# Optimization experiments

Measured on AMD Instinct MI355X. Metric: run time of the kernel, lower is better.

## Reference

```python
import jax, jax.numpy as jnp
import numpy as np

D = 256
H = 1024
N_TAU = 10  # steps per delay interval; dt = tau / N_TAU (matches dt = 0.1*tau in source)


def setup_inputs() -> dict:
    key = jax.random.key(0)
    k1, k2, k3, k4 = jax.random.split(key, 4)
    x_0 = jax.random.normal(k1, (D,), dtype=jnp.float32)
    # Small weight scales keep the explicit Euler DDE solve numerically tame over 10k steps
    W1 = jax.random.normal(k2, (H, 2 * D), dtype=jnp.float32) * 0.05
    b1 = jax.random.normal(k3, (H,), dtype=jnp.float32) * 0.05
    W2 = jax.random.normal(k4, (D, H), dtype=jnp.float32) * 0.002
    b2 = jnp.zeros((D,), dtype=jnp.float32)
    return {"x_0": x_0, "W1": W1, "b1": b1, "W2": W2, "b2": b2, "tau": 1, "T": 1000}


def reference(x_0, W1, b1, W2, b2, tau, T):
    # DDE: x'(t) = F(x(t), x(t - tau), t) for t in [0, T]; x(t) = x_0 for t in [-tau, 0].
    # Solver: explicit Euler with dt = tau / N_tau, N = floor(T / dt) steps.
    dt = 0.1 * float(tau)
    N = int(np.floor(float(T) / dt))

    def F(x, y, t):
        # MODEL: one-hidden-layer tanh MLP on concat(x(t), x(t - tau))
        h = jnp.tanh(W1 @ jnp.concatenate([x, y]) + b1)
        return W2 @ h + b2

    # Rolling buffer of the last N_tau states; history x(t) = x_0 for t <= 0.
    buf0 = jnp.broadcast_to(x_0, (N_TAU, D))  # buf[0] == x[j - N_tau]

    def step(carry, t):
        x, buf = carry
        y = buf[0]                     # delayed state x(t - tau)
        x_new = x + dt * F(x, y, t)
        buf_new = jnp.concatenate([buf[1:], x[None, :]], axis=0)
        return (x_new, buf_new), x_new

    ts = jnp.arange(N, dtype=jnp.float32) * dt
    (_, _), xs = jax.lax.scan(step, (x_0, buf0), ts)  # xs: [N, d]
    traj = jnp.concatenate([x_0[None, :], xs], axis=0)  # [N+1, d]
    return traj.T  # [d, N+1]: kth column = state at kth time step
```

## Files before the change

kernel.cpp:

```cpp
#include <hip/hip_runtime.h>
#include <math.h>


#define NTAU 10
#define DD   256
#define HH   1024
#define NWG  32
#define TPB  256
#define HPW  (HH / NWG)
#define KPT  64

__global__ __launch_bounds__(TPB, 1)
void ndde_persist(const float* __restrict__ x0,
                  const float* __restrict__ W1,
                  const float* __restrict__ b1,
                  const float* __restrict__ W2,
                  const float* __restrict__ b2,
                  const int*   __restrict__ taup,
                  float* __restrict__ out,
                  float*        P,
                  unsigned int* ctr,
                  int N)
{
    const int w  = blockIdx.x;
    const int t  = threadIdx.x;
    const int r  = t >> 3;
    const int i  = t & 7;
    const int row  = w * HPW + r;
    const int col0 = w * HPW;

    const float dt = 0.1f * (float)(*taup);

    __shared__ __align__(16) float xcur[DD];
    __shared__ __align__(16) float hist[NTAU][DD];
    __shared__ __align__(16) float hsh[HPW];

    float4 w1r[16];
    {
        const float* wrow = W1 + (size_t)row * (2 * DD);
        #pragma unroll
        for (int j = 0; j < 16; ++j) {
            int jj = (j + i) & 15;
            w1r[j] = *(const float4*)(wrow + i * KPT + 4 * jj);
        }
    }
    float4 w2r[8];
    #pragma unroll
    for (int c = 0; c < 8; ++c)
        w2r[c] = *(const float4*)(W2 + (size_t)t * HH + col0 + 4 * c);

    const float b1r = b1[row];
    const float b2r = b2[t];
    const float x0r = x0[t];
    const bool  writer = (r == w);
    float* orow = out + (size_t)t * (N + 1);

    xcur[t] = x0r;
    #pragma unroll
    for (int q = 0; q < NTAU; ++q) hist[q][t] = x0r;
    if (writer) orow[0] = x0r;
    __syncthreads();

    int hidx = 0;
    for (int s = 0; s < N; ++s) {
        const float* zbase = (i < 4) ? (xcur + (i & 3) * KPT)
                                     : (hist[hidx] + (i & 3) * KPT);
        float ax = 0.f, ay = 0.f, az = 0.f, aw = 0.f;
        #pragma unroll
        for (int j = 0; j < 16; ++j) {
            int jj = (j + i) & 15;
            float4 zv = *(const float4*)(zbase + 4 * jj);
            float4 wv = w1r[j];
            ax = fmaf(wv.x, zv.x, ax);
            ay = fmaf(wv.y, zv.y, ay);
            az = fmaf(wv.z, zv.z, az);
            aw = fmaf(wv.w, zv.w, aw);
        }
        float acc = (ax + ay) + (az + aw);
        acc += __shfl_xor(acc, 1);
        acc += __shfl_xor(acc, 2);
        acc += __shfl_xor(acc, 4);
        if (i == 0) hsh[r] = tanhf(acc + b1r);
        __syncthreads();

        float px = 0.f, py = 0.f, pz = 0.f, pw = 0.f;
        #pragma unroll
        for (int c = 0; c < 8; ++c) {
            float4 hv = *(const float4*)(&hsh[4 * c]);
            float4 wv = w2r[c];
            px = fmaf(wv.x, hv.x, px);
            py = fmaf(wv.y, hv.y, py);
            pz = fmaf(wv.z, hv.z, pz);
            pw = fmaf(wv.w, hv.w, pw);
        }
        float p = (px + py) + (pz + pw);

        float* slot = P + ((size_t)(s & 1) * NWG + w) * DD;
        __hip_atomic_store(slot + t, p, __ATOMIC_RELAXED, __HIP_MEMORY_SCOPE_AGENT);
        __syncthreads();

        if (t == 0) {
            __hip_atomic_fetch_add(ctr, 1u, __ATOMIC_RELAXED, __HIP_MEMORY_SCOPE_AGENT);
            const unsigned int target = (unsigned int)(s + 1) * NWG;
            while (__hip_atomic_load(ctr, __ATOMIC_RELAXED, __HIP_MEMORY_SCOPE_AGENT) < target)
                __builtin_amdgcn_s_sleep(1);
        }
        __syncthreads();

        float* gp = P + (size_t)(s & 1) * NWG * DD + t;
        float delta = 0.f;
        #pragma unroll
        for (int ww = 0; ww < NWG; ++ww)
            delta += __hip_atomic_load(gp + (size_t)ww * DD, __ATOMIC_RELAXED,
                                       __HIP_MEMORY_SCOPE_AGENT);

        const float xold = xcur[t];
        const float xnew = fmaf(dt, delta + b2r, xold);
        hist[hidx][t] = xold;
        xcur[t]       = xnew;
        if (writer) orow[s + 1] = xnew;
        hidx = (hidx + 1 == NTAU) ? 0 : hidx + 1;
        __syncthreads();
    }
}

extern "C" void kernel_launch(void* const* d_in, const int* in_sizes, int n_in,
                              void* d_out, int out_size, void* d_ws, size_t ws_size,
                              hipStream_t stream)
{
    const float* x0  = (const float*)d_in[0];
    const float* W1  = (const float*)d_in[1];
    const float* b1  = (const float*)d_in[2];
    const float* W2  = (const float*)d_in[3];
    const float* b2  = (const float*)d_in[4];
    const int*  taup = (const int*)d_in[5];

    const int Dv = in_sizes[0];
    const int N  = out_size / Dv - 1;

    unsigned int* ctr = (unsigned int*)d_ws;
    float* P = (float*)((char*)d_ws + 256);

    hipMemsetAsync(d_ws, 0, 256, stream);

    hipLaunchKernelGGL(ndde_persist, dim3(NWG), dim3(TPB), 0, stream,
                       x0, W1, b1, W2, b2, taup,
                       (float*)d_out, P, ctr, N);
}
```

Measured before the change: 28.50 ms.

## Replace global atomic counter barrier with step-tagged 64-bit partial slots

Each partial sum is now stored packed with its step number in a 64-bit word. Readers spin on the tags of all 32 slots directly instead of waiting on a fetch-add counter barrier and extra __syncthreads. This removes the serialized atomic counter, the single-thread spin, and two workgroup barriers per step. In exchange every thread polls 32 remote slots, and slots are never cleared between launches, so stale tags from an earlier call could match and be read as valid data.

Result: slower. 75.43 ms (+164.7%).

```diff
diff --git a/kernel.cpp b/kernel.cpp
--- a/kernel.cpp
+++ b/kernel.cpp
@@ -10,6 +10,9 @@
 #define HPW  (HH / NWG)
 #define KPT  64
 
+typedef unsigned long long u64;
+typedef unsigned int       u32;
+
 __global__ __launch_bounds__(TPB, 1)
 void ndde_persist(const float* __restrict__ x0,
                   const float* __restrict__ W1,
@@ -18,8 +21,7 @@
                   const float* __restrict__ b2,
                   const int*   __restrict__ taup,
                   float* __restrict__ out,
-                  float*        P,
-                  unsigned int* ctr,
+                  u64*          P,
                   int N)
 {
     const int w  = blockIdx.x;
@@ -95,24 +97,27 @@
         }
         float p = (px + py) + (pz + pw);
 
-        float* slot = P + ((size_t)(s & 1) * NWG + w) * DD;
-        __hip_atomic_store(slot + t, p, __ATOMIC_RELAXED, __HIP_MEMORY_SCOPE_AGENT);
-        __syncthreads();
+        const u32 tag = (u32)(s + 1);
+        u64* slot = P + ((size_t)(s & 1) * NWG + w) * DD + t;
+        const u64 pk = ((u64)tag << 32) | (u64)__float_as_uint(p);
+        __hip_atomic_store(slot, pk, __ATOMIC_RELAXED, __HIP_MEMORY_SCOPE_AGENT);
 
-        if (t == 0) {
-            __hip_atomic_fetch_add(ctr, 1u, __ATOMIC_RELAXED, __HIP_MEMORY_SCOPE_AGENT);
-            const unsigned int target = (unsigned int)(s + 1) * NWG;
-            while (__hip_atomic_load(ctr, __ATOMIC_RELAXED, __HIP_MEMORY_SCOPE_AGENT) < target)
-                __builtin_amdgcn_s_sleep(1);
+        u64* gbase = P + (size_t)(s & 1) * NWG * DD + t;
+        u64 v[NWG];
+        #pragma unroll
+        for (int ww = 0; ww < NWG; ++ww)
+            v[ww] = __hip_atomic_load(gbase + (size_t)ww * DD,
+                                      __ATOMIC_RELAXED, __HIP_MEMORY_SCOPE_AGENT);
+        #pragma unroll
+        for (int ww = 0; ww < NWG; ++ww) {
+            while (!__all((int)((u32)(v[ww] >> 32) == tag)))
+                v[ww] = __hip_atomic_load(gbase + (size_t)ww * DD,
+                                          __ATOMIC_RELAXED, __HIP_MEMORY_SCOPE_AGENT);
         }
-        __syncthreads();
-
-        float* gp = P + (size_t)(s & 1) * NWG * DD + t;
         float delta = 0.f;
         #pragma unroll
         for (int ww = 0; ww < NWG; ++ww)
-            delta += __hip_atomic_load(gp + (size_t)ww * DD, __ATOMIC_RELAXED,
-                                       __HIP_MEMORY_SCOPE_AGENT);
+            delta += __uint_as_float((u32)v[ww]);
 
         const float xold = xcur[t];
         const float xnew = fmaf(dt, delta + b2r, xold);
@@ -138,12 +143,9 @@
     const int Dv = in_sizes[0];
     const int N  = out_size / Dv - 1;
 
-    unsigned int* ctr = (unsigned int*)d_ws;
-    float* P = (float*)((char*)d_ws + 256);
-
-    hipMemsetAsync(d_ws, 0, 256, stream);
+    u64* P = (u64*)d_ws;
 
     hipLaunchKernelGGL(ndde_persist, dim3(NWG), dim3(TPB), 0, stream,
                        x0, W1, b1, W2, b2, taup,
-                       (float*)d_out, P, ctr, N);
+                       (float*)d_out, P, N);
 }
```
